# Kernel optimization log

Measured on AMD Instinct MI355X. Metric: run time of the kernel, lower is better.

Reference implementation:

```python
import jax, jax.numpy as jnp
import numpy as np

DIM = 1024
H = 16
N_OSC = 1
DT = 0.1
NUM_STEPS = 5
CAUSAL = False


def setup_inputs() -> dict:
    key = jax.random.key(0)
    ks = jax.random.split(key, 6)
    B, T, D = 2, 2048, DIM
    x = jax.random.normal(ks[0], (B, T, D), dtype=jnp.float32)
    # nn.Linear weights, stored (out, in) like torch; y = x @ W.T
    s = 1.0 / np.sqrt(D)
    Wq = jax.random.uniform(ks[1], (D, D), jnp.float32, -s, s)
    Wk = jax.random.uniform(ks[2], (D, D), jnp.float32, -s, s)
    Wv = jax.random.uniform(ks[3], (D, D), jnp.float32, -s, s)
    Wo = jax.random.uniform(ks[4], (D, D), jnp.float32, -s, s)
    omega = jax.random.normal(ks[5], (H, N_OSC), dtype=jnp.float32) * 0.1
    return {"x": x, "Wq": Wq, "Wk": Wk, "Wv": Wv, "Wo": Wo, "omega": omega}


def reference(x, Wq, Wk, Wv, Wo, omega):
    B, T, D = x.shape
    dk = D // H
    scale = 1.0 / np.sqrt(dk).astype(np.float32)
    two_pi = jnp.float32(2.0 * np.pi)

    def heads(W):
        # (B,T,D) -> (B,H,T,dk)
        return (x @ W.T).reshape(B, T, H, dk).transpose(0, 2, 1, 3)

    q = heads(Wq)
    k = heads(Wk)
    v = heads(Wv)

    # coupling J_ij = softmax_j(q_i . k_j / sqrt(dk)) -> (B,H,T,T)
    logits = jnp.einsum("bhid,bhjd->bhij", q, k) * scale
    if CAUSAL:
        mask = jnp.triu(jnp.ones((T, T), dtype=bool), k=1)
        logits = jnp.where(mask[None, None], -jnp.inf, logits)
    J = jax.nn.softmax(logits, axis=-1)

    # initial phases from v: atan2(sum of first N_OSC dims, sum of next N_OSC dims)
    phases = jnp.arctan2(
        v[..., :N_OSC].sum(-1), v[..., N_OSC:2 * N_OSC].sum(-1) + 1e-8
    )  # (B,H,T)

    # omega broadcast to (B,H,T): (H,1)->(1,H,1,1)->(B,H,T,1)->squeeze
    om = jnp.broadcast_to(omega[None, :, None, :], (B, H, T, N_OSC))[..., 0]

    def step(ph, _):
        # diff[...,i,j] = phi_i - phi_j
        diff = ph[..., :, None] - ph[..., None, :]
        coupling = (J * jnp.sin(diff)).sum(-1)
        ph = (ph + DT * (om + coupling)) % two_pi
        return ph, None

    phases, _ = jax.lax.scan(step, phases, None, length=NUM_STEPS)

    v_mod = v * jnp.cos(phases)[..., None]  # (B,H,T,dk)
    out = v_mod.transpose(0, 2, 1, 3).reshape(B, T, D) @ Wo.T
    return x + out
```

## Files before the change

### kernel.cpp

```cpp
#include <hip/hip_runtime.h>
#include <hip/hip_bf16.h>

#define B_    2
#define T_    2048
#define D_    1024
#define H_    16
#define DK_   64
#define BH_   (B_*H_)
#define M_    (B_*T_)
#define NSTEP 5
#define DT_   0.1f
#define TWO_PI_F 6.28318530717958647692f
#define JROWS 8
#define LOG2E_F 1.44269504088896340736f

typedef __attribute__((ext_vector_type(8))) short s16x8;
typedef __attribute__((ext_vector_type(4))) float f32x4;
typedef __attribute__((ext_vector_type(2))) float f32x2;

__device__ __forceinline__ unsigned short f2bf(float f) {
  unsigned int u = __float_as_uint(f);
  u += 0x7FFFu + ((u >> 16) & 1u);
  return (unsigned short)(u >> 16);
}

__device__ __forceinline__ void gload_lds16(const void* g, void* l) {
  __builtin_amdgcn_global_load_lds(
      (const __attribute__((address_space(1))) unsigned int*)g,
      (__attribute__((address_space(3))) unsigned int*)l, 16, 0, 0);
}

__device__ __forceinline__ void conv8(const float* in, unsigned short* out, int i) {
  const float4* p = (const float4*)in + (size_t)i*2;
  float4 a = p[0], b = p[1];
  s16x8 o;
  o[0]=(short)f2bf(a.x); o[1]=(short)f2bf(a.y); o[2]=(short)f2bf(a.z); o[3]=(short)f2bf(a.w);
  o[4]=(short)f2bf(b.x); o[5]=(short)f2bf(b.y); o[6]=(short)f2bf(b.z); o[7]=(short)f2bf(b.w);
  *(s16x8*)(out + (size_t)i*8) = o;
}

__global__ void conv_all(const float* __restrict__ x,
                         const float* __restrict__ wq, const float* __restrict__ wk,
                         const float* __restrict__ wv, const float* __restrict__ wo,
                         unsigned short* __restrict__ xb,
                         unsigned short* __restrict__ oq, unsigned short* __restrict__ ok,
                         unsigned short* __restrict__ ov, unsigned short* __restrict__ oo)
{
  int bid = blockIdx.x;
  if (bid < 2048) {
    conv8(x, xb, bid*256 + threadIdx.x);
  } else {
    int r = bid - 2048;
    int z = r >> 9, lb = r & 511;
    const float* in = (z==0)?wq:(z==1)?wk:(z==2)?wv:wo;
    unsigned short* out = (z==0)?oq:(z==1)?ok:(z==2)?ov:oo;
    conv8(in, out, lb*256 + threadIdx.x);
  }
}

template<int BM, int MODE>
__device__ __forceinline__ void gemm_body(const unsigned short* __restrict__ A,
    const unsigned short* __restrict__ W, void* __restrict__ outp,
    const float* __restrict__ res, float scale, int m0, int n0)
{
  constexpr int MF = BM/32;
  __shared__ unsigned short lA[BM*64];
  __shared__ unsigned short lB[128*64];
  const int t = threadIdx.x, wv = t >> 6, lane = t & 63;
  const int wm = wv >> 1, wn = wv & 1;
  const int lr = lane & 15, kg = lane >> 4;
  const int lrow = lane >> 3, sch = (lane & 7) ^ lrow;

  f32x4 acc[MF][4];
#pragma unroll
  for (int i = 0; i < MF; ++i)
#pragma unroll
    for (int j = 0; j < 4; ++j) { acc[i][j][0]=0.f; acc[i][j][1]=0.f; acc[i][j][2]=0.f; acc[i][j][3]=0.f; }

  for (int kt = 0; kt < 1024; kt += 64) {
#pragma unroll
    for (int ii = 0; ii < BM/32; ++ii) {
      const int inst = wv*(BM/32) + ii;
      const int row  = inst*8 + lrow;
      gload_lds16(A + (size_t)(m0+row)*1024 + kt + sch*8, lA + inst*512);
    }
#pragma unroll
    for (int ii = 0; ii < 4; ++ii) {
      const int inst = wv*4 + ii;
      const int row  = inst*8 + lrow;
      gload_lds16(W + (size_t)(n0+row)*1024 + kt + sch*8, lB + inst*512);
    }
    __syncthreads();

    s16x8 a0[MF], a1[MF], b0[4], b1[4];
#pragma unroll
    for (int mf = 0; mf < MF; ++mf) {
      int row = wm*(BM/2) + mf*16 + lr, s7 = row & 7;
      a0[mf] = *(const s16x8*)(lA + row*64 + ((kg^s7)*8));
      a1[mf] = *(const s16x8*)(lA + row*64 + (((kg+4)^s7)*8));
    }
#pragma unroll
    for (int nf = 0; nf < 4; ++nf) {
      int row = wn*64 + nf*16 + lr, s7 = row & 7;
      b0[nf] = *(const s16x8*)(lB + row*64 + ((kg^s7)*8));
      b1[nf] = *(const s16x8*)(lB + row*64 + (((kg+4)^s7)*8));
    }
#pragma unroll
    for (int mf = 0; mf < MF; ++mf)
#pragma unroll
      for (int nf = 0; nf < 4; ++nf) {
        acc[mf][nf] = __builtin_amdgcn_mfma_f32_16x16x32_bf16(a0[mf], b0[nf], acc[mf][nf], 0,0,0);
        acc[mf][nf] = __builtin_amdgcn_mfma_f32_16x16x32_bf16(a1[mf], b1[nf], acc[mf][nf], 0,0,0);
      }
    __syncthreads();
  }

#pragma unroll
  for (int mf = 0; mf < MF; ++mf)
#pragma unroll
    for (int nf = 0; nf < 4; ++nf)
#pragma unroll
      for (int r = 0; r < 4; ++r) {
        int grow = m0 + wm*(BM/2) + mf*16 + kg*4 + r;
        int gcol = n0 + wn*64 + nf*16 + lr;
        size_t o = (size_t)grow*1024 + gcol;
        float v = acc[mf][nf][r];
        if (MODE == 0) ((unsigned short*)outp)[o] = f2bf(v*scale);
        else           ((float*)outp)[o] = v + res[o];
      }
}

__global__ __launch_bounds__(256)
void gemm_qkv(const unsigned short* __restrict__ xb,
              const unsigned short* __restrict__ wq, const unsigned short* __restrict__ wk,
              const unsigned short* __restrict__ wv_,
              unsigned short* __restrict__ Qb, unsigned short* __restrict__ Kb,
              unsigned short* __restrict__ Vb)
{
  const int z = blockIdx.z;
  const unsigned short* W = (z==0)?wq:((z==1)?wk:wv_);
  unsigned short* O = (z==0)?Qb:((z==1)?Kb:Vb);
  const float scale = (z==0) ? 0.125f*LOG2E_F : 1.0f;
  gemm_body<128,0>(xb, W, O, nullptr, scale, blockIdx.x*128, blockIdx.y*128);
}

__global__ __launch_bounds__(256)
void gemm_o(const unsigned short* __restrict__ Ab, const unsigned short* __restrict__ wo,
            float* __restrict__ out, const float* __restrict__ x)
{
  gemm_body<64,2>(Ab, wo, out, x, 1.0f, blockIdx.x*64, blockIdx.y*128);
}

__global__ __launch_bounds__(256)
void v01_kernel(const float* __restrict__ x, const float* __restrict__ Wv,
                float* __restrict__ V01)
{
  const int wv = threadIdx.x >> 6, lane = threadIdx.x & 63;
  const int row = blockIdx.x*4 + wv;
  const float4* xr = (const float4*)(x + (size_t)row*1024);
  float4 xv[4];
#pragma unroll
  for (int p = 0; p < 4; ++p) xv[p] = xr[lane + p*64];

  float part[32];
#pragma unroll
  for (int c = 0; c < 32; ++c) {
    const int wcol = (c >> 1)*DK_ + (c & 1);
    const float4* wr = (const float4*)(Wv + (size_t)wcol*1024);
    float a = 0.f;
#pragma unroll
    for (int p = 0; p < 4; ++p) {
      float4 bv = wr[lane + p*64];
      a += xv[p].x*bv.x + xv[p].y*bv.y + xv[p].z*bv.z + xv[p].w*bv.w;
    }
    part[c] = a;
  }
#pragma unroll
  for (int c = 0; c < 32; ++c)
#pragma unroll
    for (int m = 1; m < 64; m <<= 1)
      part[c] += __shfl_xor(part[c], m);

  float outv = part[0];
#pragma unroll
  for (int c = 1; c < 32; ++c)
    if ((lane & 31) == c) outv = part[c];
  if (lane < 32) V01[(size_t)row*32 + lane] = outv;
}

__global__ void phase_init2(const float* __restrict__ V01, float* __restrict__ ph,
                            float* __restrict__ cw, float* __restrict__ sw)
{
  int idx = blockIdx.x*256 + threadIdx.x;
  int tt = idx & (T_-1);
  int bh = idx >> 11;
  int b = bh >> 4, h = bh & 15;
  float a = V01[((size_t)(b*T_ + tt))*32 + h*2 + 0];
  float c = V01[((size_t)(b*T_ + tt))*32 + h*2 + 1] + 1e-8f;
  ph[idx] = atan2f(a, c);
  float r = fmaxf(sqrtf(a*a + c*c), 1e-30f);
  cw[idx] = c / r;
  sw[idx] = a / r;
}

__global__ __launch_bounds__(256)
void build_t(const unsigned short* __restrict__ Qb, const unsigned short* __restrict__ Kb,
             unsigned char* __restrict__ J,
             const float* __restrict__ cr, const float* __restrict__ sr,
             float* __restrict__ parts)
{
  __shared__ unsigned char lds[32768];
  unsigned short* lK = (unsigned short*)lds;
  unsigned short* lQ = (unsigned short*)(lds + 16384);
  unsigned char*  lJ = lds;
  float* lRed = (float*)(lds + 16384);

  const int ib = blockIdx.x, jb = blockIdx.y, bh = blockIdx.z;
  const int b = bh >> 4, h = bh & 15;
  const int t = threadIdx.x, wv = t >> 6, lane = t & 63;
  const int wj = wv >> 1, wi = wv & 1;
  const int lr = lane & 15, kg = lane >> 4;
  const int lrow = lane >> 3, sch = (lane & 7) ^ lrow;
  const int i0 = ib*128;

  const unsigned short* Kbase = Kb + (size_t)b*T_*D_ + h*DK_;
  const unsigned short* Qbase = Qb + (size_t)b*T_*D_ + h*DK_;

#pragma unroll
  for (int ii = 0; ii < 4; ++ii) {
    const int inst = wv*4 + ii;
    const int row  = inst*8 + lrow;
    gload_lds16(Kbase + (size_t)(jb*128 + row)*D_ + sch*8, lK + inst*512);
    gload_lds16(Qbase + (size_t)(i0 + row)*D_ + sch*8, lQ + inst*512);
  }
  __syncthreads();

  s16x8 ak0[4], ak1[4], bq0[4], bq1[4];
#pragma unroll
  for (int s = 0; s < 4; ++s) {
    int row = wj*64 + s*16 + lr, s7 = row & 7;
    ak0[s] = *(const s16x8*)(lK + row*64 + ((kg^s7)*8));
    ak1[s] = *(const s16x8*)(lK + row*64 + (((kg+4)^s7)*8));
  }
#pragma unroll
  for (int ti = 0; ti < 4; ++ti) {
    int row = wi*64 + ti*16 + lr, s7 = row & 7;
    bq0[ti] = *(const s16x8*)(lQ + row*64 + ((kg^s7)*8));
    bq1[ti] = *(const s16x8*)(lQ + row*64 + (((kg+4)^s7)*8));
  }
  const float* crow = cr + (size_t)bh*T_;
  const float* srow = sr + (size_t)bh*T_;
  f32x2 cjlo[4], cjhi[4], sjlo[4], sjhi[4];
#pragma unroll
  for (int s = 0; s < 4; ++s) {
    float4 cj = *(const float4*)(crow + jb*128 + wj*64 + s*16 + kg*4);
    float4 sj = *(const float4*)(srow + jb*128 + wj*64 + s*16 + kg*4);
    cjlo[s][0]=cj.x; cjlo[s][1]=cj.y; cjhi[s][0]=cj.z; cjhi[s][1]=cj.w;
    sjlo[s][0]=sj.x; sjlo[s][1]=sj.y; sjhi[s][0]=sj.z; sjhi[s][1]=sj.w;
  }
  __syncthreads();

  f32x2 Cp2[4], Sp2[4], Ep2[4];
#pragma unroll
  for (int ti = 0; ti < 4; ++ti) {
    Cp2[ti][0]=0.f; Cp2[ti][1]=0.f; Sp2[ti][0]=0.f; Sp2[ti][1]=0.f; Ep2[ti][0]=0.f; Ep2[ti][1]=0.f;
  }
#pragma unroll
  for (int ti = 0; ti < 4; ++ti) {
    const int row = wi*64 + ti*16 + lr;
    const int rx = row & 7;
#pragma unroll
    for (int s = 0; s < 4; ++s) {
      f32x4 dd; dd[0]=0.f; dd[1]=0.f; dd[2]=0.f; dd[3]=0.f;
      dd = __builtin_amdgcn_mfma_f32_16x16x32_bf16(ak0[s], bq0[ti], dd, 0, 0, 0);
      dd = __builtin_amdgcn_mfma_f32_16x16x32_bf16(ak1[s], bq1[ti], dd, 0, 0, 0);
      float e0 = __builtin_amdgcn_exp2f(dd[0]), e1 = __builtin_amdgcn_exp2f(dd[1]);
      float e2 = __builtin_amdgcn_exp2f(dd[2]), e3 = __builtin_amdgcn_exp2f(dd[3]);
      unsigned int p = 0;
      p = __builtin_amdgcn_cvt_pk_fp8_f32(e0, e1, p, false);
      p = __builtin_amdgcn_cvt_pk_fp8_f32(e2, e3, p, true);
      *(unsigned int*)(lJ + row*128 + (((wj*4 + s) ^ rx) << 4) + kg*4) = p;
      f32x2 elo; elo[0]=e0; elo[1]=e1;
      f32x2 ehi; ehi[0]=e2; ehi[1]=e3;
      Cp2[ti] += elo*cjlo[s] + ehi*cjhi[s];
      Sp2[ti] += elo*sjlo[s] + ehi*sjhi[s];
      Ep2[ti] += elo + ehi;
    }
  }
  float Cp[4], Sp[4], Ep[4];
#pragma unroll
  for (int ti = 0; ti < 4; ++ti) {
    Cp[ti] = Cp2[ti][0] + Cp2[ti][1];
    Sp[ti] = Sp2[ti][0] + Sp2[ti][1];
    Ep[ti] = Ep2[ti][0] + Ep2[ti][1];
  }
#pragma unroll
  for (int m = 16; m < 64; m <<= 1)
#pragma unroll
    for (int ti = 0; ti < 4; ++ti) {
      Cp[ti] += __shfl_xor(Cp[ti], m);
      Sp[ti] += __shfl_xor(Sp[ti], m);
      Ep[ti] += __shfl_xor(Ep[ti], m);
    }
  if (kg == 0) {
#pragma unroll
    for (int ti = 0; ti < 4; ++ti) {
      int i = wi*64 + ti*16 + lr;
      lRed[(wj*128 + i)*3 + 0] = Cp[ti];
      lRed[(wj*128 + i)*3 + 1] = Sp[ti];
      lRed[(wj*128 + i)*3 + 2] = Ep[ti];
    }
  }
  __syncthreads();

#pragma unroll
  for (int it = 0; it < 4; ++it) {
    int row = it*32 + (t >> 3);
    int blk = t & 7;
    uint4 v = *(const uint4*)(lJ + row*128 + (((blk ^ (row & 7)) << 4)));
    *(uint4*)(J + ((size_t)(bh*T_ + i0 + row))*T_ + jb*128 + blk*16) = v;
  }
  if (parts != nullptr && t < 128) {
    float C = lRed[t*3+0] + lRed[(128+t)*3+0];
    float S = lRed[t*3+1] + lRed[(128+t)*3+1];
    float E = lRed[t*3+2] + lRed[(128+t)*3+2];
    const size_t N = (size_t)BH_*T_;
    size_t rowg = (size_t)bh*T_ + i0 + t;
    parts[(0*16 + jb)*N + rowg] = C;
    parts[(1*16 + jb)*N + rowg] = S;
    parts[(2*16 + jb)*N + rowg] = E;
  }
}

__global__ void finalize1(const float* __restrict__ parts,
                          const float* __restrict__ cr, const float* __restrict__ sr,
                          float* __restrict__ cw, float* __restrict__ sw,
                          float* __restrict__ ph, const float* __restrict__ omega)
{
  int idx = blockIdx.x*256 + threadIdx.x;
  const size_t N = (size_t)BH_*T_;
  float C = 0.f, S = 0.f, E = 0.f;
#pragma unroll
  for (int c = 0; c < 16; ++c) {
    C += parts[(0*16 + c)*N + idx];
    S += parts[(1*16 + c)*N + idx];
    E += parts[(2*16 + c)*N + idx];
  }
  int bh = idx >> 11;
  float si = sr[idx], ci = cr[idx];
  float coupling = (si*C - ci*S) / E;
  float pn = ph[idx] + DT_*(omega[bh & 15] + coupling);
  pn = fmodf(pn, TWO_PI_F);
  if (pn < 0.f) pn += TWO_PI_F;
  ph[idx] = pn;
  cw[idx] = __cosf(pn);
  sw[idx] = __sinf(pn);
}

__global__ __launch_bounds__(256)
void j_step2(const unsigned char* __restrict__ J,
             const float* __restrict__ cr, const float* __restrict__ sr,
             float* __restrict__ cw, float* __restrict__ sw,
             float* __restrict__ ph, const float* __restrict__ omega)
{
  const int wv = threadIdx.x >> 6, lane = threadIdx.x & 63;
  const int r0 = (blockIdx.x*4 + wv)*JROWS;
  const int bh = r0 >> 11;
  const float4* c4 = (const float4*)(cr + (size_t)bh*T_);
  const float4* s4 = (const float4*)(sr + (size_t)bh*T_);

  f32x2 C2[JROWS], S2[JROWS], E2[JROWS];
#pragma unroll
  for (int r = 0; r < JROWS; ++r) {
    C2[r][0]=0.f; C2[r][1]=0.f; S2[r][0]=0.f; S2[r][1]=0.f; E2[r][0]=0.f; E2[r][1]=0.f;
  }

#pragma unroll
  for (int k = 0; k < 2; ++k) {
    int idx = k*64 + lane;
    f32x2 clo[4], chi[4], slo[4], shi[4];
#pragma unroll
    for (int q = 0; q < 4; ++q) {
      float4 cv = c4[idx*4+q], sv = s4[idx*4+q];
      clo[q][0]=cv.x; clo[q][1]=cv.y; chi[q][0]=cv.z; chi[q][1]=cv.w;
      slo[q][0]=sv.x; slo[q][1]=sv.y; shi[q][0]=sv.z; shi[q][1]=sv.w;
    }
#pragma unroll
    for (int row = 0; row < JROWS; ++row) {
      uint4 jv = *(const uint4*)(J + (size_t)(r0+row)*T_ + (size_t)idx*16);
#pragma unroll
      for (int q = 0; q < 4; ++q) {
        unsigned int wq_ = (q==0)?jv.x:(q==1)?jv.y:(q==2)?jv.z:jv.w;
        f32x2 lo = __builtin_amdgcn_cvt_pk_f32_fp8(wq_, false);
        f32x2 hi = __builtin_amdgcn_cvt_pk_f32_fp8(wq_, true);
        C2[row] += lo*clo[q] + hi*chi[q];
        S2[row] += lo*slo[q] + hi*shi[q];
        E2[row] += lo + hi;
      }
    }
  }

  float C[JROWS], S[JROWS], E[JROWS];
#pragma unroll
  for (int r = 0; r < JROWS; ++r) { C[r]=C2[r][0]+C2[r][1]; S[r]=S2[r][0]+S2[r][1]; E[r]=E2[r][0]+E2[r][1]; }

#pragma unroll
  for (int m = 1; m < 64; m <<= 1) {
#pragma unroll
    for (int row = 0; row < JROWS; ++row) {
      C[row] += __shfl_xor(C[row], m);
      S[row] += __shfl_xor(S[row], m);
      E[row] += __shfl_xor(E[row], m);
    }
  }

  if (lane < JROWS) {
    float Cc = C[0], Ss = S[0], Ee = E[0];
#pragma unroll
    for (int r = 1; r < JROWS; ++r)
      if (lane == r) { Cc = C[r]; Ss = S[r]; Ee = E[r]; }
    int pidx = r0 + lane;
    float si = sr[pidx], ci = cr[pidx];
    float om = omega[bh & 15];
    float coupling = (si*Cc - ci*Ss) / Ee;
    float pn = ph[pidx] + DT_*(om + coupling);
    pn = fmodf(pn, TWO_PI_F);
    if (pn < 0.f) pn += TWO_PI_F;
    ph[pidx] = pn;
    cw[pidx] = __cosf(pn);
    sw[pidx] = __sinf(pn);
  }
}

__global__ void vmod2(unsigned short* __restrict__ V, const float* __restrict__ cfin)
{
  int idx = blockIdx.x*256 + threadIdx.x;
  int row = idx >> 7;
  int g = idx & 127;
  int h = g >> 3;
  int b = row >> 11, tt = row & 2047;
  float c = cfin[((size_t)(b*H_ + h))*T_ + tt];
  s16x8 v = *(s16x8*)(V + (size_t)idx*8);
  s16x8 o;
#pragma unroll
  for (int e = 0; e < 8; ++e) {
    float f = __uint_as_float(((unsigned int)(unsigned short)v[e]) << 16);
    o[e] = (short)f2bf(f * c);
  }
  *(s16x8*)(V + (size_t)idx*8) = o;
}

extern "C" void kernel_launch(void* const* d_in, const int* in_sizes, int n_in,
                              void* d_out, int out_size, void* d_ws, size_t ws_size,
                              hipStream_t stream)
{
  const float* x     = (const float*)d_in[0];
  const float* Wq    = (const float*)d_in[1];
  const float* Wk    = (const float*)d_in[2];
  const float* Wv    = (const float*)d_in[3];
  const float* Wo    = (const float*)d_in[4];
  const float* omega = (const float*)d_in[5];
  float* out = (float*)d_out;

  char* w = (char*)d_ws;
  unsigned short* Qb  = (unsigned short*)w; w += (size_t)M_*D_*2;
  unsigned short* Kb  = (unsigned short*)w; w += (size_t)M_*D_*2;
  unsigned short* Vb  = (unsigned short*)w; w += (size_t)M_*D_*2;
  unsigned short* wob = (unsigned short*)w; w += (size_t)D_*D_*2;
  float* ph   = (float*)w; w += (size_t)BH_*T_*4;
  float* csb[2]; float* snb[2];
  csb[0] = (float*)w; w += (size_t)BH_*T_*4;
  snb[0] = (float*)w; w += (size_t)BH_*T_*4;
  csb[1] = (float*)w; w += (size_t)BH_*T_*4;
  snb[1] = (float*)w; w += (size_t)BH_*T_*4;
  float* V01 = (float*)w; w += (size_t)M_*32*4;
  unsigned char* J = (unsigned char*)w; w += (size_t)BH_*T_*T_;
  float* parts = (float*)w; w += (size_t)3*16*BH_*T_*4;
  const bool fuse = (ws_size >= (size_t)(w - (char*)d_ws));
  unsigned short* xb  = (unsigned short*)J;
  unsigned short* wqb = (unsigned short*)(J + (size_t)M_*D_*2);
  unsigned short* wkb = wqb + (size_t)D_*D_;
  unsigned short* wvb = wkb + (size_t)D_*D_;

  conv_all<<<4096, 256, 0, stream>>>(x, Wq, Wk, Wv, Wo, xb, wqb, wkb, wvb, wob);

  gemm_qkv<<<dim3(M_/128, D_/128, 3), 256, 0, stream>>>(xb, wqb, wkb, wvb, Qb, Kb, Vb);

  v01_kernel<<<M_/4, 256, 0, stream>>>(x, Wv, V01);
  phase_init2<<<BH_*T_/256, 256, 0, stream>>>(V01, ph, csb[0], snb[0]);

  build_t<<<dim3(T_/128, T_/128, BH_), 256, 0, stream>>>(
      Qb, Kb, J, csb[0], snb[0], fuse ? parts : nullptr);

  int s0;
  if (fuse) {
    finalize1<<<BH_*T_/256, 256, 0, stream>>>(parts, csb[0], snb[0], csb[1], snb[1], ph, omega);
    s0 = 1;
  } else {
    s0 = 0;
  }
  for (int s = s0; s < NSTEP; ++s)
    j_step2<<<BH_*T_/(4*JROWS), 256, 0, stream>>>(J, csb[s&1], snb[s&1],
                                                  csb[(s+1)&1], snb[(s+1)&1], ph, omega);

  vmod2<<<M_*D_/8/256, 256, 0, stream>>>(Vb, csb[NSTEP&1]);
  gemm_o<<<dim3(M_/64, D_/128), 256, 0, stream>>>(Vb, wob, out, x);
}
```

Measured before the change: 276.8 us.

## Repartition build_t so each wave owns full row strips and writes J directly

```diff
diff --git a/kernel.cpp b/kernel.cpp
--- a/kernel.cpp
+++ b/kernel.cpp
@@ -212,16 +212,14 @@
   __shared__ unsigned char lds[32768];
   unsigned short* lK = (unsigned short*)lds;
   unsigned short* lQ = (unsigned short*)(lds + 16384);
-  unsigned char*  lJ = lds;
-  float* lRed = (float*)(lds + 16384);
 
   const int ib = blockIdx.x, jb = blockIdx.y, bh = blockIdx.z;
   const int b = bh >> 4, h = bh & 15;
   const int t = threadIdx.x, wv = t >> 6, lane = t & 63;
-  const int wj = wv >> 1, wi = wv & 1;
   const int lr = lane & 15, kg = lane >> 4;
   const int lrow = lane >> 3, sch = (lane & 7) ^ lrow;
   const int i0 = ib*128;
+  const int s7l = lr & 7;
 
   const unsigned short* Kbase = Kb + (size_t)b*T_*D_ + h*DK_;
   const unsigned short* Qbase = Qb + (size_t)b*T_*D_ + h*DK_;
@@ -235,61 +233,66 @@
   }
   __syncthreads();
 
-  s16x8 ak0[4], ak1[4], bq0[4], bq1[4];
-#pragma unroll
-  for (int s = 0; s < 4; ++s) {
-    int row = wj*64 + s*16 + lr, s7 = row & 7;
-    ak0[s] = *(const s16x8*)(lK + row*64 + ((kg^s7)*8));
-    ak1[s] = *(const s16x8*)(lK + row*64 + (((kg+4)^s7)*8));
-  }
-#pragma unroll
-  for (int ti = 0; ti < 4; ++ti) {
-    int row = wi*64 + ti*16 + lr, s7 = row & 7;
+  s16x8 bq0[2], bq1[2];
+#pragma unroll
+  for (int ti = 0; ti < 2; ++ti) {
+    int row = wv*32 + ti*16 + lr, s7 = row & 7;
     bq0[ti] = *(const s16x8*)(lQ + row*64 + ((kg^s7)*8));
     bq1[ti] = *(const s16x8*)(lQ + row*64 + (((kg+4)^s7)*8));
   }
-  const float* crow = cr + (size_t)bh*T_;
-  const float* srow = sr + (size_t)bh*T_;
-  f32x2 cjlo[4], cjhi[4], sjlo[4], sjhi[4];
-#pragma unroll
-  for (int s = 0; s < 4; ++s) {
-    float4 cj = *(const float4*)(crow + jb*128 + wj*64 + s*16 + kg*4);
-    float4 sj = *(const float4*)(srow + jb*128 + wj*64 + s*16 + kg*4);
-    cjlo[s][0]=cj.x; cjlo[s][1]=cj.y; cjhi[s][0]=cj.z; cjhi[s][1]=cj.w;
-    sjlo[s][0]=sj.x; sjlo[s][1]=sj.y; sjhi[s][0]=sj.z; sjhi[s][1]=sj.w;
-  }
   __syncthreads();
 
-  f32x2 Cp2[4], Sp2[4], Ep2[4];
-#pragma unroll
-  for (int ti = 0; ti < 4; ++ti) {
+  unsigned char* lJw = lds + 16384 + wv*4096;
+  const float* crow = cr + (size_t)bh*T_ + jb*128;
+  const float* srow = sr + (size_t)bh*T_ + jb*128;
+
+  f32x2 Cp2[2], Sp2[2], Ep2[2];
+#pragma unroll
+  for (int ti = 0; ti < 2; ++ti) {
     Cp2[ti][0]=0.f; Cp2[ti][1]=0.f; Sp2[ti][0]=0.f; Sp2[ti][1]=0.f; Ep2[ti][0]=0.f; Ep2[ti][1]=0.f;
   }
-#pragma unroll
-  for (int ti = 0; ti < 4; ++ti) {
-    const int row = wi*64 + ti*16 + lr;
-    const int rx = row & 7;
-#pragma unroll
-    for (int s = 0; s < 4; ++s) {
+
+  const int r8 = lane >> 3, blk = lane & 7;
+
+#pragma unroll
+  for (int ti = 0; ti < 2; ++ti) {
+#pragma unroll
+    for (int s = 0; s < 8; ++s) {
+      int srw = s*16 + lr;
+      s16x8 ak0 = *(const s16x8*)(lK + srw*64 + ((kg^s7l)*8));
+      s16x8 ak1 = *(const s16x8*)(lK + srw*64 + (((kg+4)^s7l)*8));
+      float4 cj = *(const float4*)(crow + s*16 + kg*4);
+      float4 sj = *(const float4*)(srow + s*16 + kg*4);
       f32x4 dd; dd[0]=0.f; dd[1]=0.f; dd[2]=0.f; dd[3]=0.f;
-      dd = __builtin_amdgcn_mfma_f32_16x16x32_bf16(ak0[s], bq0[ti], dd, 0, 0, 0);
-      dd = __builtin_amdgcn_mfma_f32_16x16x32_bf16(ak1[s], bq1[ti], dd, 0, 0, 0);
+      dd = __builtin_amdgcn_mfma_f32_16x16x32_bf16(ak0, bq0[ti], dd, 0, 0, 0);
+      dd = __builtin_amdgcn_mfma_f32_16x16x32_bf16(ak1, bq1[ti], dd, 0, 0, 0);
       float e0 = __builtin_amdgcn_exp2f(dd[0]), e1 = __builtin_amdgcn_exp2f(dd[1]);
       float e2 = __builtin_amdgcn_exp2f(dd[2]), e3 = __builtin_amdgcn_exp2f(dd[3]);
       unsigned int p = 0;
       p = __builtin_amdgcn_cvt_pk_fp8_f32(e0, e1, p, false);
       p = __builtin_amdgcn_cvt_pk_fp8_f32(e2, e3, p, true);
-      *(unsigned int*)(lJ + row*128 + (((wj*4 + s) ^ rx) << 4) + kg*4) = p;
+      *(unsigned int*)(lJw + (ti*16 + lr)*128 + (((s ^ s7l) << 4)) + kg*4) = p;
       f32x2 elo; elo[0]=e0; elo[1]=e1;
       f32x2 ehi; ehi[0]=e2; ehi[1]=e3;
-      Cp2[ti] += elo*cjlo[s] + ehi*cjhi[s];
-      Sp2[ti] += elo*sjlo[s] + ehi*sjhi[s];
+      f32x2 cl; cl[0]=cj.x; cl[1]=cj.y;  f32x2 ch; ch[0]=cj.z; ch[1]=cj.w;
+      f32x2 sl; sl[0]=sj.x; sl[1]=sj.y;  f32x2 sh; sh[0]=sj.z; sh[1]=sj.w;
+      Cp2[ti] += elo*cl + ehi*ch;
+      Sp2[ti] += elo*sl + ehi*sh;
       Ep2[ti] += elo + ehi;
     }
-  }
-  float Cp[4], Sp[4], Ep[4];
-#pragma unroll
-  for (int ti = 0; ti < 4; ++ti) {
+    asm volatile("s_waitcnt lgkmcnt(0)" ::: "memory");
+    __builtin_amdgcn_sched_barrier(0);
+#pragma unroll
+    for (int half = 0; half < 2; ++half) {
+      int row = half*8 + r8;
+      uint4 v = *(const uint4*)(lJw + (ti*16 + row)*128 + (((blk ^ (row & 7)) << 4)));
+      *(uint4*)(J + ((size_t)(bh*T_ + i0 + wv*32 + ti*16 + row))*T_ + jb*128 + blk*16) = v;
+    }
+  }
+
+  float Cp[2], Sp[2], Ep[2];
+#pragma unroll
+  for (int ti = 0; ti < 2; ++ti) {
     Cp[ti] = Cp2[ti][0] + Cp2[ti][1];
     Sp[ti] = Sp2[ti][0] + Sp2[ti][1];
     Ep[ti] = Ep2[ti][0] + Ep2[ti][1];
@@ -297,38 +300,20 @@
 #pragma unroll
   for (int m = 16; m < 64; m <<= 1)
 #pragma unroll
-    for (int ti = 0; ti < 4; ++ti) {
+    for (int ti = 0; ti < 2; ++ti) {
       Cp[ti] += __shfl_xor(Cp[ti], m);
       Sp[ti] += __shfl_xor(Sp[ti], m);
       Ep[ti] += __shfl_xor(Ep[ti], m);
     }
-  if (kg == 0) {
-#pragma unroll
-    for (int ti = 0; ti < 4; ++ti) {
-      int i = wi*64 + ti*16 + lr;
-      lRed[(wj*128 + i)*3 + 0] = Cp[ti];
-      lRed[(wj*128 + i)*3 + 1] = Sp[ti];
-      lRed[(wj*128 + i)*3 + 2] = Ep[ti];
-    }
-  }
-  __syncthreads();
-
-#pragma unroll
-  for (int it = 0; it < 4; ++it) {
-    int row = it*32 + (t >> 3);
-    int blk = t & 7;
-    uint4 v = *(const uint4*)(lJ + row*128 + (((blk ^ (row & 7)) << 4)));
-    *(uint4*)(J + ((size_t)(bh*T_ + i0 + row))*T_ + jb*128 + blk*16) = v;
-  }
-  if (parts != nullptr && t < 128) {
-    float C = lRed[t*3+0] + lRed[(128+t)*3+0];
-    float S = lRed[t*3+1] + lRed[(128+t)*3+1];
-    float E = lRed[t*3+2] + lRed[(128+t)*3+2];
+  if (parts != nullptr && kg == 0) {
     const size_t N = (size_t)BH_*T_;
-    size_t rowg = (size_t)bh*T_ + i0 + t;
-    parts[(0*16 + jb)*N + rowg] = C;
-    parts[(1*16 + jb)*N + rowg] = S;
-    parts[(2*16 + jb)*N + rowg] = E;
+#pragma unroll
+    for (int ti = 0; ti < 2; ++ti) {
+      size_t rowg = (size_t)bh*T_ + i0 + wv*32 + ti*16 + lr;
+      parts[(0*16 + jb)*N + rowg] = Cp[ti];
+      parts[(1*16 + jb)*N + rowg] = Sp[ti];
+      parts[(2*16 + jb)*N + rowg] = Ep[ti];
+    }
   }
 }
 
```

New measurement: 286.0 us. +3.3%, slower.
